# Optimization experiments

Hardware: AMD Instinct MI355X
Metric: run time of the kernel (lower is better)

The kernel has to match this reference:

```python
import jax, jax.numpy as jnp
import numpy as np

B, S, D, H = 2, 2048, 1024, 16
HD = D // H  # 64


def setup_inputs() -> dict:
    key = jax.random.key(0)
    k0, k1, k2 = jax.random.split(key, 3)
    return {
        "x": jax.random.normal(k0, (B, S, D), jnp.float32),
        "qkv_w": jax.random.normal(k1, (D, 3 * D), jnp.float32) / np.sqrt(D).astype(np.float32),
        "qkv_b": jnp.zeros((3 * D,), jnp.float32),
        "out_w": jax.random.normal(k2, (D, D), jnp.float32) / np.sqrt(D).astype(np.float32),
        "out_b": jnp.zeros((D,), jnp.float32),
    }


def reference(x, qkv_w, qkv_b, out_w, out_b):
    b, s, d = x.shape
    h, hd = H, d // H
    scale = 1.0 / np.sqrt(hd).astype(np.float32)
    # qkv projection: [b, s, 3d] -> [b, s, 3, h, hd]
    qkv = (x @ qkv_w + qkv_b).reshape(b, s, 3, h, hd)
    q, k, v = qkv[:, :, 0], qkv[:, :, 1], qkv[:, :, 2]  # each [b, s, h, hd]
    # attention logits [b, h, q, k]
    logits = jnp.einsum("bqhd,bkhd->bhqk", q, k)
    # causal mask applied before scaling (as in source; -inf is scale-invariant)
    causal_mask = jnp.triu(jnp.ones((s, s), bool), 1)
    logits = jnp.where(causal_mask, -jnp.inf, logits) * scale
    att = jax.nn.softmax(logits, axis=-1)
    out = jnp.einsum("bhqk,bkhd->bqhd", att, v).reshape(b, s, d)
    return out @ out_w + out_b
```

## Files before the change

### kernel.cpp

```cpp
#include <hip/hip_runtime.h>


typedef __bf16 bf16x8 __attribute__((ext_vector_type(8)));
typedef float f32x4 __attribute__((ext_vector_type(4)));
typedef float f32x16 __attribute__((ext_vector_type(16)));
typedef unsigned short u16;
typedef u16 u16x8 __attribute__((ext_vector_type(8)));
typedef unsigned u32x4 __attribute__((ext_vector_type(4)));

#define NEG_INF (-__builtin_inff())
#define QSCALE 0.180336880110323f
#define FIXED_M 24.0f

__device__ __forceinline__ u16 f2b(float f) {
    unsigned u = __builtin_bit_cast(unsigned, f);
    u += 0x7fffu + ((u >> 16) & 1u);
    return (u16)(u >> 16);
}

__device__ __forceinline__ unsigned cvtpk(float lo, float hi) {
    unsigned r;
    asm("v_cvt_pk_bf16_f32 %0, %1, %2" : "=v"(r) : "v"(lo), "v"(hi));
    return r;
}

__device__ __forceinline__ void plswap(unsigned &a, unsigned &b) {
    asm("v_permlane32_swap_b32 %0, %1" : "+v"(a), "+v"(b));
}

__device__ __forceinline__ void gload_lds16(const u16* g, u16* l) {
    __builtin_amdgcn_global_load_lds(
        (__attribute__((address_space(1))) unsigned int*)(g),
        (__attribute__((address_space(3))) unsigned int*)(l),
        16u, 0, 0u);
}

__device__ __forceinline__ int swzb(int u) {
    return u ^ (((u >> 7) & 7) << 4);
}

__global__ void cast_f32_bf16(const float* __restrict__ X, u16* __restrict__ Y, int n4)
{
    int i = blockIdx.x * blockDim.x + threadIdx.x;
    if (i >= n4) return;
    float4 v = ((const float4*)X)[i];
    ((ushort4*)Y)[i] = make_ushort4(f2b(v.x), f2b(v.y), f2b(v.z), f2b(v.w));
}

__global__ void transpose_cast(const float* __restrict__ W, u16* __restrict__ Wt, int K, int N)
{
    __shared__ float tile[32][33];
    const int c0 = blockIdx.x * 32, r0 = blockIdx.y * 32;
    const int tc = threadIdx.x & 31, tr = threadIdx.x >> 5;
#pragma unroll
    for (int i = 0; i < 4; ++i)
        tile[tr + i*8][tc] = W[(size_t)(r0 + tr + i*8) * N + c0 + tc];
    __syncthreads();
#pragma unroll
    for (int i = 0; i < 4; ++i) {
        int nn = tr + i*8;
        Wt[(size_t)(c0 + nn) * K + r0 + tc] = f2b(tile[tc][nn]);
    }
}

template<int MODE>
__global__ __launch_bounds__(256) void gemm_bt(
    const u16* __restrict__ A, const u16* __restrict__ Bt,
    const float* __restrict__ bias, float* __restrict__ Cf,
    u16* __restrict__ qb, u16* __restrict__ kb, u16* __restrict__ vb,
    int M, int N, int K)
{
    __shared__ __align__(16) u16 As[128 * 32];
    __shared__ __align__(16) u16 Bs[128 * 32];
    const int tid  = threadIdx.x;
    const int wave = tid >> 6, lane = tid & 63;
    const int quad = lane >> 4, l16 = lane & 15;
    const int m0 = blockIdx.y * 128, n0 = blockIdx.x * 128;
    const int wm = (wave >> 1) * 64, wn = (wave & 1) * 64;

    f32x4 acc[4][4] = {};

    for (int kt = 0; kt < K; kt += 32) {
#pragma unroll
        for (int iss = 0; iss < 2; ++iss) {
            const int e = iss * 2048 + tid * 8;
            const int row = e >> 5, col = e & 31;
            gload_lds16(A  + (size_t)(m0 + row) * K + kt + col, As + iss * 2048 + wave * 512);
            gload_lds16(Bt + (size_t)(n0 + row) * K + kt + col, Bs + iss * 2048 + wave * 512);
        }
        __syncthreads();
        bf16x8 af[4], bfr[4];
#pragma unroll
        for (int i = 0; i < 4; ++i) {
            af[i]  = *(const bf16x8*)(As + (wm + i*16 + l16) * 32 + quad * 8);
            bfr[i] = *(const bf16x8*)(Bs + (wn + i*16 + l16) * 32 + quad * 8);
        }
#pragma unroll
        for (int i = 0; i < 4; ++i)
#pragma unroll
            for (int j = 0; j < 4; ++j)
                acc[i][j] = __builtin_amdgcn_mfma_f32_16x16x32_bf16(af[i], bfr[j], acc[i][j], 0, 0, 0);
        __syncthreads();
    }

#pragma unroll
    for (int i = 0; i < 4; ++i)
#pragma unroll
        for (int j = 0; j < 4; ++j)
#pragma unroll
            for (int r = 0; r < 4; ++r) {
                const int m = m0 + wm + i*16 + quad*4 + r;
                const int n = n0 + wn + j*16 + l16;
                float v = acc[i][j][r] + bias[n];
                if (MODE == 0) {
                    Cf[(size_t)m * N + n] = v;
                } else {
                    const int t = n >> 10, h = (n >> 6) & 15, hd = n & 63;
                    const int b = m >> 11, s = m & 2047;
                    const size_t idx = ((size_t)(b * 16 + h) * 2048 + s) * 64 + hd;
                    if (t == 0)      qb[idx] = f2b(v * QSCALE);
                    else if (t == 1) kb[idx] = f2b(v);
                    else             vb[idx] = f2b(v);
                }
            }
}

__global__ __launch_bounds__(256) void transpose_v(const u16* __restrict__ vb, u16* __restrict__ vt)
{
    __shared__ u16 tile[64][72];
    const int bh = blockIdx.y, s0 = blockIdx.x * 64;
    const size_t base = (size_t)bh * (2048 * 64);
    const int r = threadIdx.x >> 3, c = (threadIdx.x & 7) * 8;
#pragma unroll
    for (int i = 0; i < 2; ++i) {
        u16x8 v = *(const u16x8*)(vb + base + (size_t)(s0 + r + i*32) * 64 + c);
        *(u16x8*)(&tile[r + i*32][c]) = v;
    }
    __syncthreads();
#pragma unroll
    for (int i = 0; i < 2; ++i) {
        const int hd = r + i*32;
        u16 tmp[8];
#pragma unroll
        for (int j = 0; j < 8; ++j) tmp[j] = tile[c + j][hd];
        *(u16x8*)(vt + base + (size_t)hd * 2048 + s0 + c) = *(u16x8*)&tmp[0];
    }
}

__global__ __launch_bounds__(256) void flash_attn(
    const u16* __restrict__ qb, const u16* __restrict__ kb, const u16* __restrict__ vt,
    u16* __restrict__ attn)
{
    __shared__ __align__(16) u16 Kl[2][4096];
    __shared__ __align__(16) u16 Vl[2][4096];
    __shared__ __align__(16) f32x16 red_of[2][2][2][64];
    __shared__ float red_li[2][2][64];
    __shared__ float al[2][2][32];

    const int tid  = threadIdx.x;
    const int wave = tid >> 6, lane = tid & 63;
    const int l31 = lane & 31, hi = lane >> 5;
    const int hi8 = hi * 8, hi4 = hi * 4;

    const int lin = (int)blockIdx.x;
    const int bh  = (lin & 7) | (((lin >> 3) & 3) << 3);
    const int g   = lin >> 5;
    const int pairsel = wave >> 1, phase = wave & 1;
    const int p   = 2 * g + pairsel;
    const size_t base = (size_t)bh * (2048 * 64);

    const int rb0 = 32 * p;
    const int rb1 = 32 * (63 - p);
    const int klo = p, khi = 63 - p;
    const int T = 32 - g;

    int koff[2], voff[2], dstw[2];
#pragma unroll
    for (int i = 0; i < 2; ++i) {
        const int u = (tid + 256 * i) * 16;
        const int ktsub = u >> 12, krow = (u >> 7) & 31;
        koff[i] = (ktsub * 32 + krow) * 64 + ((u & 127) >> 1);
        const int half = (u >> 6) & 1;
        voff[i] = (krow * 2 + half) * 2048 + ktsub * 32 + ((u & 63) >> 1);
        dstw[i] = swzb(u) >> 1;
    }
    int rdK[4], rdV[2][2];
#pragma unroll
    for (int ks = 0; ks < 4; ++ks) {
        const int u = phase * 4096 + l31 * 128 + ks * 32 + hi * 16;
        rdK[ks] = swzb(u) >> 1;
    }
#pragma unroll
    for (int c = 0; c < 2; ++c)
#pragma unroll
        for (int s2 = 0; s2 < 2; ++s2) {
            const int u = phase * 4096 + (c * 16 + (l31 >> 1)) * 128 + (l31 & 1) * 64
                        + s2 * 32 + hi * 16;
            rdV[c][s2] = swzb(u) >> 1;
        }

    bf16x8 qf[2][4];
#pragma unroll
    for (int ks = 0; ks < 4; ++ks) {
        qf[0][ks] = *(const bf16x8*)(qb + base + (size_t)(rb0 + l31) * 64 + ks*16 + hi8);
        qf[1][ks] = *(const bf16x8*)(qb + base + (size_t)(rb1 + l31) * 64 + ks*16 + hi8);
    }

    f32x16 of[2][2] = {};
    float li[2] = {0.f, 0.f};

    u16x8 rk[2], rv[2];
    auto LOADS = [&](int s) {
#pragma unroll
        for (int i = 0; i < 2; ++i) {
            rk[i] = *(const u16x8*)(kb + base + (size_t)s * 4096 + koff[i]);
            rv[i] = *(const u16x8*)(vt + base + (size_t)s * 64 + voff[i]);
        }
    };
    auto WRITES = [&](int b) {
#pragma unroll
        for (int i = 0; i < 2; ++i) {
            *(u16x8*)(&Kl[b][dstw[i]]) = rk[i];
            *(u16x8*)(&Vl[b][dstw[i]]) = rv[i];
        }
    };

    LOADS(0); WRITES(0);
    __syncthreads();

    for (int s = 0; s < T; ++s) {
        const bool pre = (s + 1 < T);
        if (pre) LOADS(s + 1);

        const int kth = 2 * s + phase;
        const int key0 = kth * 32;
        const bool a_hi = (kth <= khi), a_lo = (kth <= klo);

        if (a_hi | a_lo) {
            const int buf = s & 1;
            bf16x8 kf[4], vf[2][2];
#pragma unroll
            for (int ks = 0; ks < 4; ++ks)
                kf[ks] = *(const bf16x8*)(&Kl[buf][rdK[ks]]);
#pragma unroll
            for (int c = 0; c < 2; ++c)
#pragma unroll
                for (int s2 = 0; s2 < 2; ++s2)
                    vf[c][s2] = *(const bf16x8*)(&Vl[buf][rdV[c][s2]]);

#define PROC_TILE(TT, RB, MT)                                                    \
        do {                                                                     \
            f32x16 st;                                                           \
            _Pragma("unroll")                                                    \
            for (int r = 0; r < 16; ++r) st[r] = -FIXED_M;                       \
            __builtin_amdgcn_s_setprio(1);                                       \
            _Pragma("unroll")                                                    \
            for (int ks = 0; ks < 4; ++ks)                                       \
                st = __builtin_amdgcn_mfma_f32_32x32x16_bf16(kf[ks], qf[TT][ks], st, 0, 0, 0); \
            __builtin_amdgcn_s_setprio(0);                                       \
            const bool mt_ = (MT);                                               \
            const int lim_ = (RB) + l31 - key0;                                  \
            _Pragma("unroll")                                                    \
            for (int r = 0; r < 16; ++r) {                                       \
                float e = __builtin_exp2f(st[r]);                                \
                if (mt_ && ((r&3) + 8*(r>>2) + hi4 > lim_)) e = 0.f;             \
                st[r] = e;                                                       \
            }                                                                    \
            li[TT] += (((st[0]+st[1]) + (st[2]+st[3])) + ((st[4]+st[5]) + (st[6]+st[7]))) \
                    + (((st[8]+st[9]) + (st[10]+st[11])) + ((st[12]+st[13]) + (st[14]+st[15]))); \
            unsigned cw[8];                                                      \
            _Pragma("unroll")                                                    \
            for (int i = 0; i < 8; ++i) cw[i] = cvtpk(st[2*i], st[2*i+1]);       \
            plswap(cw[0], cw[2]); plswap(cw[1], cw[3]);                          \
            plswap(cw[4], cw[6]); plswap(cw[5], cw[7]);                          \
            bf16x8 pa[2];                                                        \
            { u32x4 t0 = {cw[0], cw[1], cw[2], cw[3]};                           \
              u32x4 t1 = {cw[4], cw[5], cw[6], cw[7]};                           \
              pa[0] = __builtin_bit_cast(bf16x8, t0);                            \
              pa[1] = __builtin_bit_cast(bf16x8, t1); }                          \
            __builtin_amdgcn_s_setprio(1);                                       \
            _Pragma("unroll")                                                    \
            for (int c = 0; c < 2; ++c) {                                        \
                of[TT][c] = __builtin_amdgcn_mfma_f32_32x32x16_bf16(pa[0], vf[c][0], of[TT][c], 0, 0, 0); \
                of[TT][c] = __builtin_amdgcn_mfma_f32_32x32x16_bf16(pa[1], vf[c][1], of[TT][c], 0, 0, 0); \
            }                                                                    \
            __builtin_amdgcn_s_setprio(0);                                       \
        } while (0)

            if (a_hi) PROC_TILE(1, rb1, kth == khi);
            if (a_lo) PROC_TILE(0, rb0, kth == klo);
#undef PROC_TILE
        }

        if (pre) WRITES((s + 1) & 1);
        __syncthreads();
    }

    if (phase) {
#pragma unroll
        for (int t = 0; t < 2; ++t) {
#pragma unroll
            for (int c = 0; c < 2; ++c)
                red_of[pairsel][t][c][lane] = of[t][c];
            red_li[pairsel][t][lane] = li[t];
        }
    }
    __syncthreads();
    if (phase) return;
#pragma unroll
    for (int t = 0; t < 2; ++t) {
#pragma unroll
        for (int c = 0; c < 2; ++c)
            of[t][c] += red_of[pairsel][t][c][lane];
        li[t] += red_li[pairsel][t][lane];
    }

#pragma unroll
    for (int t = 0; t < 2; ++t) {
        li[t] += __shfl_xor(li[t], 32);
        al[pairsel][t][l31] = li[t];
    }
    const int b = bh >> 4, h = bh & 15;
    const int rbs[2] = {rb0, rb1};
#pragma unroll
    for (int t = 0; t < 2; ++t)
#pragma unroll
        for (int gq = 0; gq < 4; ++gq) {
            const f32x4 lv = *(const f32x4*)(&al[pairsel][t][gq*8 + hi4]);
            f32x4 inv;
#pragma unroll
            for (int rr = 0; rr < 4; ++rr) inv[rr] = 1.0f / lv[rr];
#pragma unroll
            for (int c = 0; c < 2; ++c)
#pragma unroll
                for (int rr = 0; rr < 4; ++rr) {
                    const int q = rbs[t] + gq*8 + hi4 + rr;
                    u16* dst = attn + ((size_t)(b * 2048 + q)) * 1024 + h * 64 + c*32;
                    dst[l31] = f2b(of[t][c][gq*4 + rr] * inv[rr]);
                }
        }
}

extern "C" void kernel_launch(void* const* d_in, const int* in_sizes, int n_in,
                              void* d_out, int out_size, void* d_ws, size_t ws_size,
                              hipStream_t stream)
{
    const float* x     = (const float*)d_in[0];
    const float* qkv_w = (const float*)d_in[1];
    const float* qkv_b = (const float*)d_in[2];
    const float* out_w = (const float*)d_in[3];
    const float* out_b = (const float*)d_in[4];
    float* out = (float*)d_out;

    char* ws = (char*)d_ws;
    u16* qkv_wt = (u16*)ws;  ws += (size_t)3072 * 1024 * 2;
    u16* out_wt = (u16*)ws;  ws += (size_t)1024 * 1024 * 2;
    u16* xb     = (u16*)ws;  ws += (size_t)4096 * 1024 * 2;
    u16* qb     = (u16*)ws;  ws += (size_t)4096 * 1024 * 2;
    u16* kb     = (u16*)ws;  ws += (size_t)4096 * 1024 * 2;
    u16* vb     = (u16*)ws;  ws += (size_t)4096 * 1024 * 2;
    u16* vt     = (u16*)ws;

    cast_f32_bf16<<<4096, 256, 0, stream>>>(x, xb, 4096 * 1024 / 4);
    transpose_cast<<<dim3(96, 32), 256, 0, stream>>>(qkv_w, qkv_wt, 1024, 3072);
    transpose_cast<<<dim3(32, 32), 256, 0, stream>>>(out_w, out_wt, 1024, 1024);

    gemm_bt<1><<<dim3(24, 32), 256, 0, stream>>>(xb, qkv_wt, qkv_b, nullptr,
                                                 qb, kb, vb, 4096, 3072, 1024);
    transpose_v<<<dim3(32, 32), 256, 0, stream>>>(vb, vt);
    flash_attn<<<512, 256, 0, stream>>>(qb, kb, vt, xb);
    gemm_bt<0><<<dim3(8, 32), 256, 0, stream>>>(xb, out_wt, out_b, out,
                                                nullptr, nullptr, nullptr, 4096, 1024, 1024);
}
```

Measured before the change: 201.3 us.

## Double-buffer GEMM LDS tiles, remap workgroups, and tweak attention reduction layout

The GEMM kernel now double-buffers its A/B shared-memory tiles. It prefetches the next K-slice while computing the current one and keeps a single barrier per iteration. Workgroup IDs are also remapped so adjacent blocks are spread across XCDs. In the attention kernel, the score MFMA chain is seeded directly from a hoisted constant vector, and the cross-wave output reduction moves to a float-transposed LDS layout to avoid bank conflicts. The cost is doubled GEMM LDS use, which may lower occupancy.

```diff
diff --git a/kernel.cpp b/kernel.cpp
--- a/kernel.cpp
+++ b/kernel.cpp
@@ -70,30 +70,42 @@
     u16* __restrict__ qb, u16* __restrict__ kb, u16* __restrict__ vb,
     int M, int N, int K)
 {
-    __shared__ __align__(16) u16 As[128 * 32];
-    __shared__ __align__(16) u16 Bs[128 * 32];
+    __shared__ __align__(16) u16 As[2][128 * 32];
+    __shared__ __align__(16) u16 Bs[2][128 * 32];
     const int tid  = threadIdx.x;
     const int wave = tid >> 6, lane = tid & 63;
     const int quad = lane >> 4, l16 = lane & 15;
-    const int m0 = blockIdx.y * 128, n0 = blockIdx.x * 128;
+
+    const int nx = gridDim.x, nwg = nx * gridDim.y;
+    int wg = blockIdx.y * nx + blockIdx.x;
+    wg = (wg & 7) * (nwg >> 3) + (wg >> 3);
+    const int m0 = (wg / nx) * 128, n0 = (wg % nx) * 128;
     const int wm = (wave >> 1) * 64, wn = (wave & 1) * 64;
 
     f32x4 acc[4][4] = {};
 
-    for (int kt = 0; kt < K; kt += 32) {
+    auto stage = [&](int buf, int kt) {
 #pragma unroll
         for (int iss = 0; iss < 2; ++iss) {
             const int e = iss * 2048 + tid * 8;
             const int row = e >> 5, col = e & 31;
-            gload_lds16(A  + (size_t)(m0 + row) * K + kt + col, As + iss * 2048 + wave * 512);
-            gload_lds16(Bt + (size_t)(n0 + row) * K + kt + col, Bs + iss * 2048 + wave * 512);
-        }
-        __syncthreads();
+            gload_lds16(A  + (size_t)(m0 + row) * K + kt + col, &As[buf][iss * 2048 + wave * 512]);
+            gload_lds16(Bt + (size_t)(n0 + row) * K + kt + col, &Bs[buf][iss * 2048 + wave * 512]);
+        }
+    };
+
+    stage(0, 0);
+    __syncthreads();
+
+    int buf = 0;
+    for (int kt = 0; kt < K; kt += 32) {
+        if (kt + 32 < K) stage(buf ^ 1, kt + 32);
+
         bf16x8 af[4], bfr[4];
 #pragma unroll
         for (int i = 0; i < 4; ++i) {
-            af[i]  = *(const bf16x8*)(As + (wm + i*16 + l16) * 32 + quad * 8);
-            bfr[i] = *(const bf16x8*)(Bs + (wn + i*16 + l16) * 32 + quad * 8);
+            af[i]  = *(const bf16x8*)(&As[buf][(wm + i*16 + l16) * 32 + quad * 8]);
+            bfr[i] = *(const bf16x8*)(&Bs[buf][(wn + i*16 + l16) * 32 + quad * 8]);
         }
 #pragma unroll
         for (int i = 0; i < 4; ++i)
@@ -101,6 +113,7 @@
             for (int j = 0; j < 4; ++j)
                 acc[i][j] = __builtin_amdgcn_mfma_f32_16x16x32_bf16(af[i], bfr[j], acc[i][j], 0, 0, 0);
         __syncthreads();
+        buf ^= 1;
     }
 
 #pragma unroll
@@ -153,7 +166,7 @@
 {
     __shared__ __align__(16) u16 Kl[2][4096];
     __shared__ __align__(16) u16 Vl[2][4096];
-    __shared__ __align__(16) f32x16 red_of[2][2][2][64];
+    __shared__ float red_f[2][2][2][16][64];
     __shared__ float red_li[2][2][64];
     __shared__ float al[2][2][32];
 
@@ -206,6 +219,10 @@
         qf[1][ks] = *(const bf16x8*)(qb + base + (size_t)(rb1 + l31) * 64 + ks*16 + hi8);
     }
 
+    f32x16 minit;
+#pragma unroll
+    for (int r = 0; r < 16; ++r) minit[r] = -FIXED_M;
+
     f32x16 of[2][2] = {};
     float li[2] = {0.f, 0.f};
 
@@ -250,12 +267,10 @@
 
 #define PROC_TILE(TT, RB, MT)                                                    \
         do {                                                                     \
-            f32x16 st;                                                           \
+            __builtin_amdgcn_s_setprio(1);                                       \
+            f32x16 st = __builtin_amdgcn_mfma_f32_32x32x16_bf16(kf[0], qf[TT][0], minit, 0, 0, 0); \
             _Pragma("unroll")                                                    \
-            for (int r = 0; r < 16; ++r) st[r] = -FIXED_M;                       \
-            __builtin_amdgcn_s_setprio(1);                                       \
-            _Pragma("unroll")                                                    \
-            for (int ks = 0; ks < 4; ++ks)                                       \
+            for (int ks = 1; ks < 4; ++ks)                                       \
                 st = __builtin_amdgcn_mfma_f32_32x32x16_bf16(kf[ks], qf[TT][ks], st, 0, 0, 0); \
             __builtin_amdgcn_s_setprio(0);                                       \
             const bool mt_ = (MT);                                               \
@@ -301,7 +316,9 @@
         for (int t = 0; t < 2; ++t) {
 #pragma unroll
             for (int c = 0; c < 2; ++c)
-                red_of[pairsel][t][c][lane] = of[t][c];
+#pragma unroll
+                for (int i = 0; i < 16; ++i)
+                    red_f[pairsel][t][c][i][lane] = of[t][c][i];
             red_li[pairsel][t][lane] = li[t];
         }
     }
@@ -311,7 +328,9 @@
     for (int t = 0; t < 2; ++t) {
 #pragma unroll
         for (int c = 0; c < 2; ++c)
-            of[t][c] += red_of[pairsel][t][c][lane];
+#pragma unroll
+            for (int i = 0; i < 16; ++i)
+                of[t][c][i] += red_f[pairsel][t][c][i][lane];
         li[t] += red_li[pairsel][t][lane];
     }
 
```

Measured after the change: 194.0 us. 1.04x faster.
